# Performance work log

Measured on AMD Instinct MI355X. Metric: run time of the kernel, lower is better.

Reference implementation:

```python
import jax, jax.numpy as jnp
import numpy as np
import math

B, S, E, H, DFF = 8, 1024, 1024, 16, 4096
HD = E // H
EPS = 1e-05


def setup_inputs() -> dict:
    key = jax.random.key(0)
    ks = jax.random.split(key, 8)
    wb_attn = math.sqrt(3.0 / E)
    wb1 = math.sqrt(3.0 * 2.0 / E)      # kaiming for linear1 (in=E)
    wb2 = math.sqrt(3.0 * 2.0 / DFF)    # kaiming for linear2 (in=DFF)
    return {
        "x": jax.random.normal(ks[0], (B, S, E), jnp.float32),
        "in_weights": jax.random.uniform(ks[1], (3, E, E), jnp.float32, -wb_attn, wb_attn),
        "out_weights": jax.random.uniform(ks[2], (E, E), jnp.float32, -wb_attn, wb_attn),
        "ln1_scale": jnp.ones((E,), jnp.float32),
        "ln1_bias": jnp.zeros((E,), jnp.float32),
        "ln2_scale": jnp.ones((E,), jnp.float32),
        "ln2_bias": jnp.zeros((E,), jnp.float32),
        "w1": jax.random.uniform(ks[3], (DFF, E), jnp.float32, -wb1, wb1),
        "b1": jnp.zeros((DFF,), jnp.float32),
        "w2": jax.random.uniform(ks[4], (E, DFF), jnp.float32, -wb2, wb2),
        "b2": jnp.zeros((E,), jnp.float32),
    }


def _layernorm(x, scale, bias):
    mean = jnp.mean(x, axis=-1, keepdims=True)
    var = jnp.var(x, axis=-1, keepdims=True, ddof=1)  # torch.var unbiased=True
    return scale * (x - mean) / jnp.sqrt(var + EPS) + bias


def reference(x, in_weights, out_weights, ln1_scale, ln1_bias, ln2_scale, ln2_bias, w1, b1, w2, b2):
    # QKV projections: note key uses in_weights[0], query [1], value [2]
    def proj(w):  # (B,S,E) -> (B,H,S,HD)
        return (x @ w).reshape(B, S, H, HD).transpose(0, 2, 1, 3)
    k = proj(in_weights[0])
    q = proj(in_weights[1])
    v = proj(in_weights[2])
    scores = jnp.einsum("bhsd,bhtd->bhst", q, k) / math.sqrt(HD)
    probs = jax.nn.softmax(scores, axis=-1)
    attn = jnp.einsum("bhst,bhtd->bhsd", probs, v).transpose(0, 2, 1, 3).reshape(B, S, E)
    attn_out = attn @ out_weights
    # quirk preserved: residual is attn_out + dropout(attn_out) = 2*attn_out (eval mode)
    x1 = _layernorm(attn_out + attn_out, ln1_scale, ln1_bias)
    ffn = jax.nn.relu(x1 @ w1.T + b1) @ w2.T + b2
    return _layernorm(x1 + ffn, ln2_scale, ln2_bias)
```

## Files before the change

kernel.cpp:

```cpp
#include <hip/hip_runtime.h>

#define E_DIM 1024
#define S_LEN 1024
#define H_NUM 16
#define HD_DIM 64
#define B_NUM 8
#define DFF_DIM 4096
#define NROWS 8192
#define QKV_LD 3072

typedef unsigned short u16;
typedef unsigned u32;
typedef short bf16v8 __attribute__((ext_vector_type(8)));
typedef float f32x4 __attribute__((ext_vector_type(4)));
typedef float f32x16 __attribute__((ext_vector_type(16)));

#define QK_SCALE 0.18033688011112042f

__device__ __forceinline__ u16 f2b(float f) {
  union { float f; unsigned u; } x; x.f = f;
  return (u16)((x.u + 0x7fffu + ((x.u >> 16) & 1u)) >> 16);
}

__device__ __forceinline__ float b2f(u16 v) {
  union { unsigned u; float f; } x; x.u = ((unsigned)v) << 16; return x.f;
}

__device__ __forceinline__ float max3f(float a, float b, float c) {
  return fmaxf(fmaxf(a, b), c);
}

__device__ __forceinline__ void gload16(const void* g, void* l) {
  __builtin_amdgcn_global_load_lds((const __attribute__((address_space(1))) void*)g,
                                   (__attribute__((address_space(3))) void*)l, 16, 0, 0);
}

template<int MODE>
__global__ __launch_bounds__(512, 2) void gemm8(
    const u16* __restrict__ A, const u16* __restrict__ Bt,
    void* __restrict__ C0, void* __restrict__ C1, const float* __restrict__ bias,
    int N, int KA, int nxt, int NT) {
  __shared__ u16 sA[2 * 16384];
  __shared__ u16 sB[2 * 16384];

  const int tid = threadIdx.x;
  const int lane = tid & 63;
  const int wid = tid >> 6;
  const int wm = wid >> 2, wn = wid & 3;
  const int l15 = lane & 15, l4 = lane >> 4;
  const int pk0 = l4 ^ (l15 & 7);

  const int gx = gridDim.x;
  const int lin = blockIdx.y * gx + blockIdx.x;
  const int chunk = (gx * gridDim.y) >> 3;
  const int xcd = lin & 7;
  const int q = lin >> 3;
  const int rpx = chunk / gx;
  const int bym = xcd * rpx + (q % rpx);
  const int bxm = q / rpx;
  const int kh = (bxm >= nxt) ? 1 : 0;
  const int bm = bym * 256;
  const int bn = (bxm - kh * nxt) * 256;
  const int k0 = kh * NT * 64;

  const int srow = tid >> 3;
  const int gch = ((tid & 7) ^ (srow & 7)) * 8;
  const u16* Ag[4];
  const u16* Bg[4];
#pragma unroll
  for (int i = 0; i < 4; ++i) {
    Ag[i] = A + k0 + (size_t)(bm + i * 64 + srow) * KA + gch;
    Bg[i] = Bt + k0 + (size_t)(bn + i * 64 + srow) * KA + gch;
  }
  const int t8 = tid * 8;

#define ST1(tile, li)                                                              \
  do {                                                                             \
    if ((li) < 4) gload16(Ag[li] + (tile) * 64, sA + ((tile)&1) * 16384 + (li)*4096 + t8); \
    else gload16(Bg[(li)-4] + (tile) * 64, sB + ((tile)&1) * 16384 + ((li)-4) * 4096 + t8); \
  } while (0)
#define STG8(tile)                                         \
  if ((tile) < NT) {                                       \
    _Pragma("unroll") for (int li = 0; li < 8; ++li) ST1(tile, li); \
  }

  bf16v8 a[4][2], b[4][2];
  f32x4 acc[8][4];
#pragma unroll
  for (int m = 0; m < 8; ++m)
#pragma unroll
    for (int n = 0; n < 4; ++n) acc[m][n] = (f32x4){0.f, 0.f, 0.f, 0.f};

#define LDA(mh, buf)                                                        \
  {                                                                         \
    _Pragma("unroll") for (int mp = 0; mp < 4; ++mp) {                      \
      const u16* rp = (buf) + (size_t)(wm * 128 + (mh)*64 + mp * 16 + l15) * 64; \
      a[mp][0] = *(const bf16v8*)(rp + pk0 * 8);                            \
      a[mp][1] = *(const bf16v8*)(rp + (pk0 ^ 4) * 8);                      \
    }                                                                       \
  }
#define LDB(n0, buf)                                                        \
  {                                                                         \
    _Pragma("unroll") for (int nn = (n0); nn < (n0) + 2; ++nn) {            \
      const u16* rp = (buf) + (size_t)(wn * 64 + nn * 16 + l15) * 64;       \
      b[nn][0] = *(const bf16v8*)(rp + pk0 * 8);                            \
      b[nn][1] = *(const bf16v8*)(rp + (pk0 ^ 4) * 8);                      \
    }                                                                       \
  }
#define MMPH(mh, n0)                                                                      \
  {                                                                                       \
    __builtin_amdgcn_s_setprio(1);                                                        \
    _Pragma("unroll") for (int mp = 0; mp < 4; ++mp) {                                    \
      _Pragma("unroll") for (int nn = (n0); nn < (n0) + 2; ++nn) {                        \
        acc[(mh)*4 + mp][nn] = __builtin_amdgcn_mfma_f32_16x16x32_bf16(                   \
            a[mp][0], b[nn][0], acc[(mh)*4 + mp][nn], 0, 0, 0);                           \
        acc[(mh)*4 + mp][nn] = __builtin_amdgcn_mfma_f32_16x16x32_bf16(                   \
            a[mp][1], b[nn][1], acc[(mh)*4 + mp][nn], 0, 0, 0);                           \
      }                                                                                   \
    }                                                                                     \
    __builtin_amdgcn_s_setprio(0);                                                        \
  }

  STG8(0);
  STG8(1);
  __builtin_amdgcn_sched_barrier(0);
  asm volatile("s_waitcnt vmcnt(8)" ::: "memory");
  __builtin_amdgcn_s_barrier();
  LDA(0, sA);
  LDB(0, sB);

  for (int t = 0; t < NT; ++t) {
    u16* sAc = sA + (t & 1) * 16384;
    u16* sBc = sB + (t & 1) * 16384;
    u16* sAn = sA + ((t + 1) & 1) * 16384;
    u16* sBn = sB + ((t + 1) & 1) * 16384;
    MMPH(0, 0);
    LDB(2, sBc);
    __builtin_amdgcn_s_barrier();
    MMPH(0, 2);
    LDA(1, sAc);
    __builtin_amdgcn_s_barrier();
    STG8(t + 2);
    MMPH(1, 0);
    __builtin_amdgcn_sched_barrier(0);
    if (t + 2 < NT)      asm volatile("s_waitcnt vmcnt(8)" ::: "memory");
    else if (t + 1 < NT) asm volatile("s_waitcnt vmcnt(0)" ::: "memory");
    __builtin_amdgcn_s_barrier();
    MMPH(1, 2);
    if (t + 1 < NT) {
      LDA(0, sAn);
      LDB(0, sBn);
    }
    __builtin_amdgcn_s_barrier();
  }

  const int lrow0 = bm + wm * 128 + l4 * 4;
  const int lcol0 = bn + wn * 64 + l15;
  const float scl = (MODE == 0 && ((bn >> 10) == 1)) ? QK_SCALE : 1.f;
  u16* Cw = (u16*)(kh ? C1 : C0);
#pragma unroll
  for (int m = 0; m < 8; ++m) {
#pragma unroll
    for (int n = 0; n < 4; ++n) {
      const int col = lcol0 + n * 16;
      float bv = 0.f;
      if (MODE == 2) bv = bias[col];
      if (MODE == 3) bv = kh ? 0.f : bias[col];
#pragma unroll
      for (int i = 0; i < 4; ++i) {
        const int row = lrow0 + m * 16 + i;
        float v = acc[m][n][i] + bv;
        if (MODE == 2) v = fmaxf(v, 0.f);
        if (MODE == 0) v *= scl;
        Cw[(size_t)row * N + col] = f2b(v);
      }
    }
  }
#undef ST1
#undef STG8
#undef LDA
#undef LDB
#undef MMPH
}

#define MKPF(dst, A0, B0, C0, D0)                                             \
  {                                                                           \
    u32 sa = (u32)__shfl_xor((int)(A0), 32), sb = (u32)__shfl_xor((int)(B0), 32); \
    u32 sc = (u32)__shfl_xor((int)(C0), 32), sd = (u32)__shfl_xor((int)(D0), 32); \
    union { u32 u[4]; bf16v8 v; } cc;                                         \
    cc.u[0] = hi ? sc : (A0); cc.u[1] = hi ? sd : (B0);                       \
    cc.u[2] = hi ? (C0) : sa; cc.u[3] = hi ? (D0) : sb;                       \
    dst = cc.v;                                                               \
  }

__device__ __forceinline__ void vt_write64(u16* sVtBuf, int4 wv, int vr, int s8) {
  int4 w2;
  w2.x = __shfl_xor(wv.x, 8); w2.y = __shfl_xor(wv.y, 8);
  w2.z = __shfl_xor(wv.z, 8); w2.w = __shfl_xor(wv.w, 8);
  const int t = vr >> 1;
  const int odd = vr & 1;
  const u16* own = (const u16*)&wv;
  const u16* par = (const u16*)&w2;
  char* dstbase = (char*)sVtBuf + (t >> 2) * 1024 + (t & 3) * 4;
#pragma unroll
  for (int k = 0; k < 4; k++) {
    const unsigned lo = odd ? (unsigned)par[4 + k] : (unsigned)own[k];
    const unsigned h2 = odd ? (unsigned)own[4 + k] : (unsigned)par[k];
    const int d = s8 * 8 + k + (odd ? 4 : 0);
    const int dsw = d ^ s8;
    *(unsigned*)(dstbase + dsw * 16) = lo | (h2 << 16);
  }
}

__global__ __launch_bounds__(512, 4) void attn_fa(
    const u16* __restrict__ qkv, u16* __restrict__ attn) {
  __shared__ u16 sK[2][64 * 64];
  __shared__ u16 sVt[2][64 * 64];

  const int tid = threadIdx.x, lane = tid & 63;
  const int l31 = lane & 31, hi = lane >> 5;
  const int w = ((blockIdx.x & 7) << 6) + (blockIdx.x >> 3);
  const int bh = w >> 2;
  const int b = bh >> 4, h = bh & 15;
  const int qrow0 = (w & 3) * 256 + (tid >> 6) * 32;
  const size_t rowb = (size_t)b * S_LEN * QKV_LD;
  const u16* kg = qkv + rowb + h * HD_DIM;
  const u16* qg = qkv + rowb + 1024 + h * HD_DIM;
  const u16* vg = qkv + rowb + 2048 + h * HD_DIM;
  const size_t obase = (size_t)b * (S_LEN * E_DIM) + (size_t)h * HD_DIM;

  bf16v8 qf[4];
#pragma unroll
  for (int ks = 0; ks < 4; ++ks)
    qf[ks] = *(const bf16v8*)(qg + (size_t)(qrow0 + l31) * QKV_LD + ks * 16 + hi * 8);

  const int kr = tid >> 3;
  const int s8 = tid & 7;
  const u16* kgsrc = kg + (size_t)kr * QKV_LD + ((s8 ^ (kr & 7)) * 8);
  const u16* vgsrc = vg + (size_t)kr * QKV_LD + s8 * 8;

  f32x16 accT[2];
#pragma unroll
  for (int i = 0; i < 16; ++i) { accT[0][i] = 0.f; accT[1][i] = 0.f; }
  float mrun = -1e30f, lrun = 0.f;

  gload16(kgsrc, sK[0] + tid * 8);
  {
    int4 v0 = *(const int4*)(vgsrc);
    vt_write64(sVt[0], v0, kr, s8);
  }
  __syncthreads();

  for (int t = 0; t < 16; ++t) {
    const int cur = t & 1;
    int4 vreg;
    if (t < 15) {
      gload16(kgsrc + (size_t)(t + 1) * 64 * QKV_LD, sK[cur ^ 1] + tid * 8);
      vreg = *(const int4*)(vgsrc + (size_t)(t + 1) * 64 * QKV_LD);
    }

    f32x16 T0, T1;
#pragma unroll
    for (int i = 0; i < 16; ++i) { T0[i] = 0.f; T1[i] = 0.f; }
#pragma unroll
    for (int ks = 0; ks < 4; ++ks) {
      const int ch = ((2 * ks + hi) ^ (l31 & 7)) * 8;
      const bf16v8 k0 = *(const bf16v8*)(sK[cur] + (size_t)l31 * 64 + ch);
      const bf16v8 k1 = *(const bf16v8*)(sK[cur] + (size_t)(32 + l31) * 64 + ch);
      T0 = __builtin_amdgcn_mfma_f32_32x32x16_bf16(k0, qf[ks], T0, 0, 0, 0);
      T1 = __builtin_amdgcn_mfma_f32_32x32x16_bf16(k1, qf[ks], T1, 0, 0, 0);
    }

    float ma = fmaxf(T0[0], T0[1]);
#pragma unroll
    for (int r = 2; r < 16; r += 2) ma = max3f(ma, T0[r], T0[r + 1]);
    float mb = fmaxf(T1[0], T1[1]);
#pragma unroll
    for (int r = 2; r < 16; r += 2) mb = max3f(mb, T1[r], T1[r + 1]);
    float mx = fmaxf(ma, mb);
    mx = fmaxf(mx, __shfl_xor(mx, 32));
    const bool skip = __all(mx <= mrun + 8.f);
    const float mnew = skip ? mrun : fmaxf(mrun, mx);
    float rs = 0.f;
#pragma unroll
    for (int r = 0; r < 16; ++r) { T0[r] = exp2f(T0[r] - mnew); rs += T0[r]; }
#pragma unroll
    for (int r = 0; r < 16; ++r) { T1[r] = exp2f(T1[r] - mnew); rs += T1[r]; }
    if (skip) {
      lrun += rs;
    } else {
      const float esc = exp2f(mrun - mnew);
      mrun = mnew;
      lrun = lrun * esc + rs;
#pragma unroll
      for (int r = 0; r < 16; ++r) { accT[0][r] *= esc; accT[1][r] *= esc; }
    }

    u32 P0[8], P1[8];
#pragma unroll
    for (int wd = 0; wd < 8; ++wd) {
      asm("v_cvt_pk_bf16_f32 %0, %1, %2" : "=v"(P0[wd]) : "v"(T0[2 * wd]), "v"(T0[2 * wd + 1]));
      asm("v_cvt_pk_bf16_f32 %0, %1, %2" : "=v"(P1[wd]) : "v"(T1[2 * wd]), "v"(T1[2 * wd + 1]));
    }
    bf16v8 pf[4];
    MKPF(pf[0], P0[0], P0[1], P0[2], P0[3]);
    MKPF(pf[1], P0[4], P0[5], P0[6], P0[7]);
    MKPF(pf[2], P1[0], P1[1], P1[2], P1[3]);
    MKPF(pf[3], P1[4], P1[5], P1[6], P1[7]);

#pragma unroll
    for (int dblk = 0; dblk < 2; ++dblk) {
      const int dd = dblk * 32 + l31;
      const int drow = (dd ^ (dd >> 3)) * 8;
#pragma unroll
      for (int ks = 0; ks < 4; ++ks) {
        const bf16v8 va = *(const bf16v8*)(sVt[cur] + (2 * ks + hi) * 512 + drow);
        accT[dblk] = __builtin_amdgcn_mfma_f32_32x32x16_bf16(va, pf[ks], accT[dblk], 0, 0, 0);
      }
    }

    if (t < 15) vt_write64(sVt[cur ^ 1], vreg, kr, s8);
    __syncthreads();
  }

  lrun += __shfl_xor(lrun, 32);
  const float linv = 1.f / lrun;
  u16* orow = attn + obase + (size_t)(qrow0 + l31) * E_DIM;
#pragma unroll
  for (int dblk = 0; dblk < 2; ++dblk)
#pragma unroll
    for (int a4 = 0; a4 < 4; ++a4) {
      ushort4 st;
      st.x = f2b(accT[dblk][4 * a4 + 0] * linv);
      st.y = f2b(accT[dblk][4 * a4 + 1] * linv);
      st.z = f2b(accT[dblk][4 * a4 + 2] * linv);
      st.w = f2b(accT[dblk][4 * a4 + 3] * linv);
      *(ushort4*)(orow + dblk * 32 + a4 * 8 + hi * 4) = st;
    }
}

template<int MODE>
__global__ __launch_bounds__(256) void ln_b16(
    const u16* __restrict__ a, const u16* __restrict__ b, const u16* __restrict__ c,
    const float* __restrict__ scale, const float* __restrict__ bias,
    float* __restrict__ outf, u16* __restrict__ outb) {
  const int row = blockIdx.x;
  const int tid = threadIdx.x;
  const size_t off = (size_t)row * 1024 + tid * 4;
  ushort4 av = *(const ushort4*)(a + off);
  ushort4 bv = *(const ushort4*)(b + off);
  float4 v;
  v.x = b2f(av.x) + b2f(bv.x);
  v.y = b2f(av.y) + b2f(bv.y);
  v.z = b2f(av.z) + b2f(bv.z);
  v.w = b2f(av.w) + b2f(bv.w);
  if (MODE == 0) {
    v.x *= 2.f; v.y *= 2.f; v.z *= 2.f; v.w *= 2.f;
  } else {
    ushort4 cv = *(const ushort4*)(c + off);
    v.x += b2f(cv.x); v.y += b2f(cv.y); v.z += b2f(cv.z); v.w += b2f(cv.w);
  }
  float s = v.x + v.y + v.z + v.w;
  float q = v.x * v.x + v.y * v.y + v.z * v.z + v.w * v.w;
#pragma unroll
  for (int o = 1; o < 64; o <<= 1) { s += __shfl_xor(s, o); q += __shfl_xor(q, o); }
  __shared__ float red[8];
  const int wave = tid >> 6, lane = tid & 63;
  if (lane == 0) { red[wave] = s; red[4 + wave] = q; }
  __syncthreads();
  s = red[0] + red[1] + red[2] + red[3];
  q = red[4] + red[5] + red[6] + red[7];
  const float mean = s * (1.f / 1024.f);
  const float var = (q - 1024.f * mean * mean) * (1.f / 1023.f);
  const float rstd = rsqrtf(var + 1e-5f);
  const int cc = tid * 4;
  float4 sc = *(const float4*)(scale + cc);
  float4 bi = *(const float4*)(bias + cc);
  float4 o;
  o.x = sc.x * (v.x - mean) * rstd + bi.x;
  o.y = sc.y * (v.y - mean) * rstd + bi.y;
  o.z = sc.z * (v.z - mean) * rstd + bi.z;
  o.w = sc.w * (v.w - mean) * rstd + bi.w;
  if (MODE == 0) {
    ushort4 ob;
    ob.x = f2b(o.x); ob.y = f2b(o.y); ob.z = f2b(o.z); ob.w = f2b(o.w);
    *(ushort4*)(outb + off) = ob;
  } else {
    *(float4*)(outf + off) = o;
  }
}

__global__ __launch_bounds__(256) void cast_bf16_k(const float* __restrict__ in,
                                                   u16* __restrict__ out, int n4) {
  const int i = blockIdx.x * blockDim.x + threadIdx.x;
  if (i >= n4) return;
  float4 v = *(const float4*)(in + (size_t)i * 4);
  ushort4 o;
  o.x = f2b(v.x); o.y = f2b(v.y); o.z = f2b(v.z); o.w = f2b(v.w);
  *(ushort4*)(out + (size_t)i * 4) = o;
}

__global__ __launch_bounds__(256) void transpose_cast_k(const float* __restrict__ in,
                                                        u16* __restrict__ out) {
  __shared__ float tile[32][33];
  const int tx = threadIdx.x & 31, ty = threadIdx.x >> 5;
  const int bx = blockIdx.x * 32, by = blockIdx.y * 32;
#pragma unroll
  for (int j = 0; j < 4; j++)
    tile[ty + j * 8][tx] = in[(size_t)(by + ty + j * 8) * 1024 + bx + tx];
  __syncthreads();
#pragma unroll
  for (int j = 0; j < 4; j++)
    out[(size_t)(bx + ty + j * 8) * 1024 + by + tx] = f2b(tile[tx][ty + j * 8]);
}

extern "C" void kernel_launch(void* const* d_in, const int* in_sizes, int n_in,
                              void* d_out, int out_size, void* d_ws, size_t ws_size,
                              hipStream_t stream) {
  const float* x    = (const float*)d_in[0];
  const float* in_w = (const float*)d_in[1];
  const float* out_w = (const float*)d_in[2];
  const float* ln1s = (const float*)d_in[3];
  const float* ln1b = (const float*)d_in[4];
  const float* ln2s = (const float*)d_in[5];
  const float* ln2b = (const float*)d_in[6];
  const float* w1   = (const float*)d_in[7];
  const float* b1   = (const float*)d_in[8];
  const float* w2   = (const float*)d_in[9];
  const float* b2   = (const float*)d_in[10];
  float* outp = (float*)d_out;

  char* ws = (char*)d_ws;
  u16*   xb    = (u16*)(ws + 0);
  u16*   qkv   = (u16*)(ws + 16777216);
  u16*   attnb = (u16*)(ws + 0);
  u16*   wo0   = (u16*)(ws + 67108864);
  u16*   wo1   = (u16*)(ws + 83886080);
  u16*   x1b   = (u16*)(ws + 100663296);
  u16*   Hb    = (u16*)(ws + 0);
  u16*   ffn0b = (u16*)(ws + 67108864);
  u16*   ffn1b = (u16*)(ws + 83886080);
  u16*   wkt   = (u16*)(ws + 150994944);
  u16*   wot   = wkt + 3145728;
  u16*   w1b   = wot + 1048576;
  u16*   w2b   = w1b + 4194304;
  (void)ws_size; (void)in_sizes; (void)n_in; (void)out_size;

  cast_bf16_k<<<8192, 256, 0, stream>>>(x, xb, 2097152);
  cast_bf16_k<<<4096, 256, 0, stream>>>(w1, w1b, 1048576);
  cast_bf16_k<<<4096, 256, 0, stream>>>(w2, w2b, 1048576);
  dim3 tg(32, 32);
  transpose_cast_k<<<tg, 256, 0, stream>>>(in_w + 0,       wkt);
  transpose_cast_k<<<tg, 256, 0, stream>>>(in_w + 1048576, wkt + 1048576);
  transpose_cast_k<<<tg, 256, 0, stream>>>(in_w + 2097152, wkt + 2097152);
  transpose_cast_k<<<tg, 256, 0, stream>>>(out_w,          wot);

  gemm8<0><<<dim3(12, 32), 512, 0, stream>>>(xb, wkt, qkv, nullptr, nullptr, 3072, 1024, 12, 16);

  attn_fa<<<512, 512, 0, stream>>>(qkv, attnb);

  gemm8<1><<<dim3(8, 32), 512, 0, stream>>>(attnb, wot, wo0, wo1, nullptr, 1024, 1024, 4, 8);

  ln_b16<0><<<8192, 256, 0, stream>>>(wo0, wo1, nullptr, ln1s, ln1b, nullptr, x1b);

  gemm8<2><<<dim3(16, 32), 512, 0, stream>>>(x1b, w1b, Hb, nullptr, b1, 4096, 1024, 16, 16);

  gemm8<3><<<dim3(8, 32), 512, 0, stream>>>(Hb, w2b, ffn0b, ffn1b, b2, 1024, 4096, 4, 32);

  ln_b16<1><<<8192, 256, 0, stream>>>(x1b, ffn0b, ffn1b, ln2s, ln2b, outp, nullptr);
}
```

Measured before the change: 343.7 us.

## Shrink GEMM tiles to 128x128 and raise occupancy to four blocks

Changes the bf16 GEMM block tile from 256x256 to 128x128 with a 64-wide K step, halving LDS buffers and cutting per-warp accumulators to 4x2 MFMA tiles. Launch bounds move to four blocks per CU, the grid dimensions quadruple, and the intra-iteration phase pipeline is simplified to a single load-then-compute step per K tile. The aim is more resident waves to hide latency and better CU fill. In exchange, per-tile data reuse drops and global/LDS traffic per FLOP roughly doubles.

```diff
diff --git a/kernel.cpp b/kernel.cpp
--- a/kernel.cpp
+++ b/kernel.cpp
@@ -36,12 +36,12 @@
 }
 
 template<int MODE>
-__global__ __launch_bounds__(512, 2) void gemm8(
+__global__ __launch_bounds__(512, 4) void gemm8(
     const u16* __restrict__ A, const u16* __restrict__ Bt,
     void* __restrict__ C0, void* __restrict__ C1, const float* __restrict__ bias,
     int N, int KA, int nxt, int NT) {
-  __shared__ u16 sA[2 * 16384];
-  __shared__ u16 sB[2 * 16384];
+  __shared__ u16 sA[2 * 8192];
+  __shared__ u16 sB[2 * 8192];
 
   const int tid = threadIdx.x;
   const int lane = tid & 63;
@@ -59,109 +59,87 @@
   const int bym = xcd * rpx + (q % rpx);
   const int bxm = q / rpx;
   const int kh = (bxm >= nxt) ? 1 : 0;
-  const int bm = bym * 256;
-  const int bn = (bxm - kh * nxt) * 256;
+  const int bm = bym * 128;
+  const int bn = (bxm - kh * nxt) * 128;
   const int k0 = kh * NT * 64;
 
   const int srow = tid >> 3;
   const int gch = ((tid & 7) ^ (srow & 7)) * 8;
-  const u16* Ag[4];
-  const u16* Bg[4];
-#pragma unroll
-  for (int i = 0; i < 4; ++i) {
-    Ag[i] = A + k0 + (size_t)(bm + i * 64 + srow) * KA + gch;
-    Bg[i] = Bt + k0 + (size_t)(bn + i * 64 + srow) * KA + gch;
-  }
+  const u16* Ag0 = A + k0 + (size_t)(bm + srow) * KA + gch;
+  const u16* Ag1 = A + k0 + (size_t)(bm + 64 + srow) * KA + gch;
+  const u16* Bg0 = Bt + k0 + (size_t)(bn + srow) * KA + gch;
+  const u16* Bg1 = Bt + k0 + (size_t)(bn + 64 + srow) * KA + gch;
   const int t8 = tid * 8;
 
-#define ST1(tile, li)                                                              \
-  do {                                                                             \
-    if ((li) < 4) gload16(Ag[li] + (tile) * 64, sA + ((tile)&1) * 16384 + (li)*4096 + t8); \
-    else gload16(Bg[(li)-4] + (tile) * 64, sB + ((tile)&1) * 16384 + ((li)-4) * 4096 + t8); \
-  } while (0)
-#define STG8(tile)                                         \
-  if ((tile) < NT) {                                       \
-    _Pragma("unroll") for (int li = 0; li < 8; ++li) ST1(tile, li); \
-  }
-
-  bf16v8 a[4][2], b[4][2];
-  f32x4 acc[8][4];
-#pragma unroll
-  for (int m = 0; m < 8; ++m)
-#pragma unroll
-    for (int n = 0; n < 4; ++n) acc[m][n] = (f32x4){0.f, 0.f, 0.f, 0.f};
-
-#define LDA(mh, buf)                                                        \
+#define ST4(tile)                                                       \
+  if ((tile) < NT) {                                                    \
+    gload16(Ag0 + (tile) * 64, sA + ((tile)&1) * 8192 + t8);            \
+    gload16(Ag1 + (tile) * 64, sA + ((tile)&1) * 8192 + 4096 + t8);     \
+    gload16(Bg0 + (tile) * 64, sB + ((tile)&1) * 8192 + t8);            \
+    gload16(Bg1 + (tile) * 64, sB + ((tile)&1) * 8192 + 4096 + t8);     \
+  }
+
+  bf16v8 a[4][2], b[2][2];
+  f32x4 acc[4][2];
+#pragma unroll
+  for (int m = 0; m < 4; ++m)
+#pragma unroll
+    for (int n = 0; n < 2; ++n) acc[m][n] = (f32x4){0.f, 0.f, 0.f, 0.f};
+
+#define LDALL(tile)                                                         \
   {                                                                         \
+    u16* bufA = sA + ((tile)&1) * 8192;                                     \
+    u16* bufB = sB + ((tile)&1) * 8192;                                     \
     _Pragma("unroll") for (int mp = 0; mp < 4; ++mp) {                      \
-      const u16* rp = (buf) + (size_t)(wm * 128 + (mh)*64 + mp * 16 + l15) * 64; \
+      const u16* rp = bufA + (size_t)(wm * 64 + mp * 16 + l15) * 64;        \
       a[mp][0] = *(const bf16v8*)(rp + pk0 * 8);                            \
       a[mp][1] = *(const bf16v8*)(rp + (pk0 ^ 4) * 8);                      \
     }                                                                       \
-  }
-#define LDB(n0, buf)                                                        \
-  {                                                                         \
-    _Pragma("unroll") for (int nn = (n0); nn < (n0) + 2; ++nn) {            \
-      const u16* rp = (buf) + (size_t)(wn * 64 + nn * 16 + l15) * 64;       \
+    _Pragma("unroll") for (int nn = 0; nn < 2; ++nn) {                      \
+      const u16* rp = bufB + (size_t)(wn * 32 + nn * 16 + l15) * 64;        \
       b[nn][0] = *(const bf16v8*)(rp + pk0 * 8);                            \
       b[nn][1] = *(const bf16v8*)(rp + (pk0 ^ 4) * 8);                      \
     }                                                                       \
   }
-#define MMPH(mh, n0)                                                                      \
-  {                                                                                       \
-    __builtin_amdgcn_s_setprio(1);                                                        \
-    _Pragma("unroll") for (int mp = 0; mp < 4; ++mp) {                                    \
-      _Pragma("unroll") for (int nn = (n0); nn < (n0) + 2; ++nn) {                        \
-        acc[(mh)*4 + mp][nn] = __builtin_amdgcn_mfma_f32_16x16x32_bf16(                   \
-            a[mp][0], b[nn][0], acc[(mh)*4 + mp][nn], 0, 0, 0);                           \
-        acc[(mh)*4 + mp][nn] = __builtin_amdgcn_mfma_f32_16x16x32_bf16(                   \
-            a[mp][1], b[nn][1], acc[(mh)*4 + mp][nn], 0, 0, 0);                           \
-      }                                                                                   \
-    }                                                                                     \
-    __builtin_amdgcn_s_setprio(0);                                                        \
-  }
-
-  STG8(0);
-  STG8(1);
+#define MM16()                                                              \
+  {                                                                         \
+    __builtin_amdgcn_s_setprio(1);                                          \
+    _Pragma("unroll") for (int mp = 0; mp < 4; ++mp) {                      \
+      _Pragma("unroll") for (int nn = 0; nn < 2; ++nn) {                    \
+        acc[mp][nn] = __builtin_amdgcn_mfma_f32_16x16x32_bf16(              \
+            a[mp][0], b[nn][0], acc[mp][nn], 0, 0, 0);                      \
+        acc[mp][nn] = __builtin_amdgcn_mfma_f32_16x16x32_bf16(              \
+            a[mp][1], b[nn][1], acc[mp][nn], 0, 0, 0);                      \
+      }                                                                     \
+    }                                                                       \
+    __builtin_amdgcn_s_setprio(0);                                          \
+  }
+
+  ST4(0);
+  ST4(1);
   __builtin_amdgcn_sched_barrier(0);
-  asm volatile("s_waitcnt vmcnt(8)" ::: "memory");
+  asm volatile("s_waitcnt vmcnt(4)" ::: "memory");
   __builtin_amdgcn_s_barrier();
-  LDA(0, sA);
-  LDB(0, sB);
 
   for (int t = 0; t < NT; ++t) {
-    u16* sAc = sA + (t & 1) * 16384;
-    u16* sBc = sB + (t & 1) * 16384;
-    u16* sAn = sA + ((t + 1) & 1) * 16384;
-    u16* sBn = sB + ((t + 1) & 1) * 16384;
-    MMPH(0, 0);
-    LDB(2, sBc);
+    LDALL(t);
     __builtin_amdgcn_s_barrier();
-    MMPH(0, 2);
-    LDA(1, sAc);
-    __builtin_amdgcn_s_barrier();
-    STG8(t + 2);
-    MMPH(1, 0);
+    ST4(t + 2);
+    MM16();
     __builtin_amdgcn_sched_barrier(0);
-    if (t + 2 < NT)      asm volatile("s_waitcnt vmcnt(8)" ::: "memory");
+    if (t + 2 < NT)      asm volatile("s_waitcnt vmcnt(4)" ::: "memory");
     else if (t + 1 < NT) asm volatile("s_waitcnt vmcnt(0)" ::: "memory");
     __builtin_amdgcn_s_barrier();
-    MMPH(1, 2);
-    if (t + 1 < NT) {
-      LDA(0, sAn);
-      LDB(0, sBn);
-    }
-    __builtin_amdgcn_s_barrier();
-  }
-
-  const int lrow0 = bm + wm * 128 + l4 * 4;
-  const int lcol0 = bn + wn * 64 + l15;
+  }
+
+  const int lrow0 = bm + wm * 64 + l4 * 4;
+  const int lcol0 = bn + wn * 32 + l15;
   const float scl = (MODE == 0 && ((bn >> 10) == 1)) ? QK_SCALE : 1.f;
   u16* Cw = (u16*)(kh ? C1 : C0);
 #pragma unroll
-  for (int m = 0; m < 8; ++m) {
-#pragma unroll
-    for (int n = 0; n < 4; ++n) {
+  for (int m = 0; m < 4; ++m) {
+#pragma unroll
+    for (int n = 0; n < 2; ++n) {
       const int col = lcol0 + n * 16;
       float bv = 0.f;
       if (MODE == 2) bv = bias[col];
@@ -176,11 +154,9 @@
       }
     }
   }
-#undef ST1
-#undef STG8
-#undef LDA
-#undef LDB
-#undef MMPH
+#undef ST4
+#undef LDALL
+#undef MM16
 }
 
 #define MKPF(dst, A0, B0, C0, D0)                                             \
@@ -455,17 +431,17 @@
   transpose_cast_k<<<tg, 256, 0, stream>>>(in_w + 2097152, wkt + 2097152);
   transpose_cast_k<<<tg, 256, 0, stream>>>(out_w,          wot);
 
-  gemm8<0><<<dim3(12, 32), 512, 0, stream>>>(xb, wkt, qkv, nullptr, nullptr, 3072, 1024, 12, 16);
+  gemm8<0><<<dim3(24, 64), 512, 0, stream>>>(xb, wkt, qkv, nullptr, nullptr, 3072, 1024, 24, 16);
 
   attn_fa<<<512, 512, 0, stream>>>(qkv, attnb);
 
-  gemm8<1><<<dim3(8, 32), 512, 0, stream>>>(attnb, wot, wo0, wo1, nullptr, 1024, 1024, 4, 8);
+  gemm8<1><<<dim3(16, 64), 512, 0, stream>>>(attnb, wot, wo0, wo1, nullptr, 1024, 1024, 8, 8);
 
   ln_b16<0><<<8192, 256, 0, stream>>>(wo0, wo1, nullptr, ln1s, ln1b, nullptr, x1b);
 
-  gemm8<2><<<dim3(16, 32), 512, 0, stream>>>(x1b, w1b, Hb, nullptr, b1, 4096, 1024, 16, 16);
-
-  gemm8<3><<<dim3(8, 32), 512, 0, stream>>>(Hb, w2b, ffn0b, ffn1b, b2, 1024, 4096, 4, 32);
+  gemm8<2><<<dim3(32, 64), 512, 0, stream>>>(x1b, w1b, Hb, nullptr, b1, 4096, 1024, 32, 16);
+
+  gemm8<3><<<dim3(16, 64), 512, 0, stream>>>(Hb, w2b, ffn0b, ffn1b, b2, 1024, 4096, 8, 32);
 
   ln_b16<1><<<8192, 256, 0, stream>>>(x1b, ffn0b, ffn1b, ln2s, ln2b, outp, nullptr);
 }
```

New measurement: 353.0 us. 1.03x slower.
